# Kernel tuning notes

Hardware: AMD Instinct MI355X
Metric: run time of the kernel (lower is better)

## Reference

```python
import jax, jax.numpy as jnp
import numpy as np

B, SQ, SK, D = 8, 2048, 2048, 256

def setup_inputs() -> dict:
    key = jax.random.key(0)
    ks = jax.random.split(key, 8)
    x1 = jax.random.normal(ks[0], (B, SQ, D), dtype=jnp.float32)
    x2 = jax.random.normal(ks[1], (B, SK, D), dtype=jnp.float32)
    x3 = jax.random.normal(ks[2], (B, SK, D), dtype=jnp.float32)  # unused by the original forward (value=x3 is dead)
    mask = jax.random.bernoulli(ks[3], 0.8, (B, SK))
    scale = 0.02
    Wq = jax.random.normal(ks[4], (D, D), dtype=jnp.float32) * scale
    Wk = jax.random.normal(ks[5], (D, D), dtype=jnp.float32) * scale
    Wv = jax.random.normal(ks[6], (D, D), dtype=jnp.float32) * scale
    bq = jnp.zeros((D,), jnp.float32)
    bk = jnp.zeros((D,), jnp.float32)
    bv = jnp.zeros((D,), jnp.float32)
    return {"x1": x1, "x2": x2, "x3": x3, "Wq": Wq, "Wk": Wk, "Wv": Wv,
            "bq": bq, "bk": bk, "bv": bv, "mask": mask}

def reference(x1, x2, x3, Wq, Wk, Wv, bq, bk, bv, mask):
    d = x1.shape[-1]
    inv_sqrt_d = 1.0 / jnp.sqrt(jnp.asarray(d, x1.dtype))
    # Projections (single-head MHA with query scaling, as in torch MHA internals)
    q = (x1 @ Wq + bq) * inv_sqrt_d          # [B, SQ, D]
    k = x2 @ Wk + bk                          # [B, SK, D]
    v = x2 @ Wv + bv                          # forward_value(key): value projected from key input
    # Raw scores
    qk = jnp.einsum('bqd,bkd->bqk', q, k)     # [B, SQ, SK]
    # Mask-derived per-column rescale: qk /= (mask.size(0)/mask.sum(-2))**0.5
    m = mask.astype(qk.dtype)                 # [B, SK]
    col_count = jnp.sum(m, axis=0, keepdims=True)           # [1, SK]
    factor = jnp.sqrt(jnp.asarray(mask.shape[0], qk.dtype) / col_count)  # [1, SK]
    qk = qk / factor                          # broadcast over [B, SQ, SK]; div-by-inf -> 0 where column count is 0
    attn = jax.nn.softmax(qk, axis=-1)
    # dropout is identity in eval / p=0
    out = jnp.einsum('bqk,bkd->bqd', attn, v)  # [B, SQ, D]
    return out
```

## Files before the change

kernel.cpp:

```cpp
#include <hip/hip_runtime.h>
#include <hip/hip_bf16.h>
#include <math.h>

#define B_  8
#define SQ_ 2048
#define SK_ 2048
#define D_  256
#define NSPLIT 4
#define KEYS_PER_SPLIT (SK_ / NSPLIT)
#define NT (KEYS_PER_SPLIT / 32)

typedef __attribute__((ext_vector_type(8))) short bf16x8;
typedef __attribute__((ext_vector_type(4))) float f32x4;
typedef __attribute__((ext_vector_type(4))) unsigned short u16x4;
typedef __attribute__((ext_vector_type(8))) _Float16 f16x8;

static __device__ __forceinline__ unsigned short f2bf(float f) {
    unsigned int u = __builtin_bit_cast(unsigned int, f);
    u += 0x7FFFu + ((u >> 16) & 1u);
    return (unsigned short)(u >> 16);
}

static __device__ __forceinline__ void gld_lds16(const unsigned short* g, unsigned short* l) {
    __builtin_amdgcn_global_load_lds(
        (const __attribute__((address_space(1))) unsigned int*)g,
        (__attribute__((address_space(3))) unsigned int*)l, 16, 0, 0);
}

__global__ void prep_kernel(const float* __restrict__ Wq, const float* __restrict__ Wk,
                            const float* __restrict__ Wv, const int* __restrict__ mask,
                            unsigned short* __restrict__ wT, float* __restrict__ r) {
    int bid = blockIdx.x;
    if (bid < 768) {
        int p = bid >> 8, k = bid & 255, n = threadIdx.x;
        const float* W = (p == 0 ? Wq : (p == 1 ? Wk : Wv));
        wT[(size_t)p * D_ * D_ + (size_t)n * D_ + k] = f2bf(W[(size_t)k * D_ + n]);
    } else {
        int s = (bid - 768) * 256 + threadIdx.x;
        float c = 0.f;
#pragma unroll
        for (int b = 0; b < B_; b++) c += (mask[b * SK_ + s] != 0) ? 1.f : 0.f;
        r[s] = sqrtf(c * 0.125f);
    }
}

__global__ __launch_bounds__(256) void proj_kernel(
    const float* __restrict__ x1, const float* __restrict__ x2,
    const float* __restrict__ bq, const float* __restrict__ bk, const float* __restrict__ bv,
    const unsigned short* __restrict__ wT, const float* __restrict__ r,
    unsigned short* __restrict__ qb, unsigned short* __restrict__ kb,
    unsigned short* __restrict__ vt)
{
    __shared__ unsigned short xs[64][264];
    __shared__ unsigned short wsh[256][36];
    const int tid = threadIdx.x;
    const int mt = blockIdx.x, b = blockIdx.y, p = blockIdx.z;
    const int m0 = mt * 64;
    const float* x = (p == 0 ? x1 : x2) + (size_t)b * SQ_ * D_;

#pragma unroll
    for (int i = 0; i < 16; i++) {
        int id = tid + i * 256;
        int row = id >> 6, c4 = id & 63;
        float4 v = *(const float4*)(x + (size_t)(m0 + row) * D_ + c4 * 4);
        u16x4 u;
        u.x = f2bf(v.x); u.y = f2bf(v.y); u.z = f2bf(v.z); u.w = f2bf(v.w);
        *(u16x4*)(&xs[row][c4 * 4]) = u;
    }

    const int wv = tid >> 6, lane = tid & 63, l15 = lane & 15, quad = lane >> 4;
    const unsigned short* w = wT + (size_t)p * D_ * D_ + (size_t)tid * D_;

    f32x4 acc[4][4];
#pragma unroll
    for (int a = 0; a < 4; a++)
#pragma unroll
        for (int n = 0; n < 4; n++) acc[a][n] = (f32x4){0.f, 0.f, 0.f, 0.f};

    bf16x8 Wreg[4];
#pragma unroll
    for (int j = 0; j < 4; j++) Wreg[j] = *(const bf16x8*)(w + j * 8);

    for (int c = 0; c < 8; c++) {
        __syncthreads();
#pragma unroll
        for (int j = 0; j < 4; j++) *(bf16x8*)(&wsh[tid][j * 8]) = Wreg[j];
        if (c < 7) {
#pragma unroll
            for (int j = 0; j < 4; j++) Wreg[j] = *(const bf16x8*)(w + (c + 1) * 32 + j * 8);
        }
        __syncthreads();

        bf16x8 af[4];
#pragma unroll
        for (int a = 0; a < 4; a++)
            af[a] = *(const bf16x8*)(&xs[a * 16 + l15][c * 32 + quad * 8]);
#pragma unroll
        for (int nt = 0; nt < 4; nt++) {
            bf16x8 bfr = *(const bf16x8*)(&wsh[wv * 64 + nt * 16 + l15][quad * 8]);
#pragma unroll
            for (int a = 0; a < 4; a++)
                acc[a][nt] = __builtin_amdgcn_mfma_f32_16x16x32_bf16(af[a], bfr, acc[a][nt], 0, 0, 0);
        }
    }

    const float* bias = (p == 0 ? bq : (p == 1 ? bk : bv));
    if (p == 2) {
#pragma unroll
        for (int nt = 0; nt < 4; nt++) {
            int d = wv * 64 + nt * 16 + l15;
            float bb = bias[d];
#pragma unroll
            for (int a = 0; a < 4; a++) {
                int seqb = m0 + a * 16 + quad * 4;
                u16x4 u;
#pragma unroll
                for (int g = 0; g < 4; g++) u[g] = f2bf(acc[a][nt][g] + bb);
                *(u16x4*)(vt + ((size_t)b * D_ + d) * SK_ + seqb) = u;
            }
        }
    } else {
        unsigned short* dst = (p == 0 ? qb : kb);
#pragma unroll
        for (int a = 0; a < 4; a++) {
            int seqb = m0 + a * 16 + quad * 4;
            float rv[4];
#pragma unroll
            for (int g = 0; g < 4; g++)
                rv[g] = (p == 1) ? r[seqb + g] : 0.0625f;
#pragma unroll
            for (int nt = 0; nt < 4; nt++) {
                int col = wv * 64 + nt * 16 + l15;
                float bb = bias[col];
#pragma unroll
                for (int g = 0; g < 4; g++) {
                    float v = (acc[a][nt][g] + bb) * rv[g];
                    dst[((size_t)b * SQ_ + seqb + g) * D_ + col] = f2bf(v);
                }
            }
        }
    }
}

__global__ __launch_bounds__(256, 2) void flash_kernel(
    const unsigned short* __restrict__ qb, const unsigned short* __restrict__ kb,
    const unsigned short* __restrict__ vt, _Float16* __restrict__ Op,
    float* __restrict__ lp)
{
    __shared__ unsigned short Ks[2][32 * 256];
    __shared__ unsigned short Vs[2][256 * 32];
    __shared__ unsigned short Ps[4][32][40];
    const int tid = threadIdx.x;
    const int wv = tid >> 6, lane = tid & 63, l15 = lane & 15, quad = lane >> 4;
    const int bid = blockIdx.x;
    const int g = bid & 31, q = bid >> 5;
    const int b = g >> 2, sp = g & 3;
    const int q0 = q * 128 + wv * 32;

    const unsigned short* kbb = kb + ((size_t)b * SK_ + sp * KEYS_PER_SPLIT) * D_;
    const unsigned short* vtb = vt + (size_t)b * D_ * SK_ + sp * KEYS_PER_SPLIT;

    int krow[4], kck[4], vd[4], vch[4];
#pragma unroll
    for (int i = 0; i < 4; i++) {
        int id = i * 256 + tid;
        krow[i] = id >> 5; kck[i] = (id & 31) ^ (krow[i] & 7);
        vd[i] = id >> 2;   vch[i] = id & 3;
    }

#pragma unroll
    for (int i = 0; i < 4; i++)
        gld_lds16(kbb + (size_t)krow[i] * D_ + kck[i] * 8,
                  &Ks[0][(i * 256 + wv * 64) * 8]);
#pragma unroll
    for (int i = 0; i < 4; i++)
        gld_lds16(vtb + (size_t)vd[i] * SK_ + vch[i] * 8,
                  &Vs[0][(i * 256 + wv * 64) * 8]);

    bf16x8 qf[2][8];
#pragma unroll
    for (int mt = 0; mt < 2; mt++) {
        const unsigned short* qrow = qb + ((size_t)(b * SQ_ + q0 + mt * 16 + l15)) * D_;
#pragma unroll
        for (int c = 0; c < 8; c++)
            qf[mt][c] = *(const bf16x8*)(qrow + c * 32 + quad * 8);
    }

    f32x4 o[2][16];
#pragma unroll
    for (int mt = 0; mt < 2; mt++)
#pragma unroll
        for (int n = 0; n < 16; n++) o[mt][n] = (f32x4){0.f, 0.f, 0.f, 0.f};
    float l_[2][4] = {{0.f, 0.f, 0.f, 0.f}, {0.f, 0.f, 0.f, 0.f}};

    for (int kt = 0; kt < NT; kt++) {
        const int cur = kt & 1;
        __syncthreads();
        if (kt + 1 < NT) {
            const unsigned short* kn = kbb + (size_t)(kt + 1) * 32 * D_;
            const unsigned short* vn = vtb + (size_t)(kt + 1) * 32;
#pragma unroll
            for (int i = 0; i < 4; i++)
                gld_lds16(kn + (size_t)krow[i] * D_ + kck[i] * 8,
                          &Ks[cur ^ 1][(i * 256 + wv * 64) * 8]);
#pragma unroll
            for (int i = 0; i < 4; i++)
                gld_lds16(vn + (size_t)vd[i] * SK_ + vch[i] * 8,
                          &Vs[cur ^ 1][(i * 256 + wv * 64) * 8]);
        }

        f32x4 s[2][2];
        s[0][0] = (f32x4){0.f,0.f,0.f,0.f}; s[0][1] = (f32x4){0.f,0.f,0.f,0.f};
        s[1][0] = (f32x4){0.f,0.f,0.f,0.f}; s[1][1] = (f32x4){0.f,0.f,0.f,0.f};
#pragma unroll
        for (int h = 0; h < 2; h++)
#pragma unroll
            for (int c = 0; c < 8; c++) {
                bf16x8 kf = *(const bf16x8*)(
                    &Ks[cur][(h * 16 + l15) * 256 + (((c * 4 + quad) ^ (l15 & 7)) * 8)]);
                s[0][h] = __builtin_amdgcn_mfma_f32_16x16x32_bf16(qf[0][c], kf, s[0][h], 0, 0, 0);
                s[1][h] = __builtin_amdgcn_mfma_f32_16x16x32_bf16(qf[1][c], kf, s[1][h], 0, 0, 0);
            }

#pragma unroll
        for (int mt = 0; mt < 2; mt++)
#pragma unroll
            for (int h = 0; h < 2; h++)
#pragma unroll
                for (int g2 = 0; g2 < 4; g2++) {
                    float pv = __expf(s[mt][h][g2]);
                    l_[mt][g2] += pv;
                    Ps[wv][mt * 16 + quad * 4 + g2][h * 16 + l15] = f2bf(pv);
                }
        asm volatile("s_waitcnt lgkmcnt(0)" ::: "memory");

        bf16x8 pf0 = *(const bf16x8*)(&Ps[wv][l15][quad * 8]);
        bf16x8 pf1 = *(const bf16x8*)(&Ps[wv][16 + l15][quad * 8]);

#pragma unroll
        for (int n = 0; n < 16; n++) {
            bf16x8 vf = *(const bf16x8*)(&Vs[cur][(n * 16 + l15) * 32 + quad * 8]);
            o[0][n] = __builtin_amdgcn_mfma_f32_16x16x32_bf16(pf0, vf, o[0][n], 0, 0, 0);
            o[1][n] = __builtin_amdgcn_mfma_f32_16x16x32_bf16(pf1, vf, o[1][n], 0, 0, 0);
        }
    }

#pragma unroll
    for (int mt = 0; mt < 2; mt++)
#pragma unroll
        for (int g2 = 0; g2 < 4; g2++) {
            float t = l_[mt][g2];
            t += __shfl_xor(t, 1, 64);
            t += __shfl_xor(t, 2, 64);
            t += __shfl_xor(t, 4, 64);
            t += __shfl_xor(t, 8, 64);
            l_[mt][g2] = t;
        }

    _Float16* op = Op + ((size_t)(sp * B_ + b) * SQ_ + q0) * D_;
#pragma unroll
    for (int mt = 0; mt < 2; mt++)
#pragma unroll
        for (int g2 = 0; g2 < 4; g2++) {
            size_t ro = (size_t)(mt * 16 + quad * 4 + g2) * D_ + l15;
#pragma unroll
            for (int n = 0; n < 16; n++)
                op[ro + n * 16] = (_Float16)(o[mt][n][g2]);
        }
    if (l15 == 0) {
        float* lpp = lp + (size_t)(sp * B_ + b) * SQ_ + q0;
#pragma unroll
        for (int mt = 0; mt < 2; mt++)
#pragma unroll
            for (int g2 = 0; g2 < 4; g2++)
                lpp[mt * 16 + quad * 4 + g2] = l_[mt][g2];
    }
}

__global__ __launch_bounds__(256) void combine_kernel(
    const _Float16* __restrict__ Op, const float* __restrict__ lp,
    float* __restrict__ out)
{
    const int gid = blockIdx.x * 256 + threadIdx.x;
    const int row = gid >> 5;
    const size_t base = (size_t)gid * 8;
    float l = lp[row] + lp[B_ * SQ_ + row] + lp[2 * B_ * SQ_ + row] + lp[3 * B_ * SQ_ + row];
    float inv = 1.f / l;
    float acc[8] = {0,0,0,0,0,0,0,0};
#pragma unroll
    for (int sp = 0; sp < NSPLIT; sp++) {
        f16x8 v = *(const f16x8*)(Op + (size_t)sp * B_ * SQ_ * D_ + base);
#pragma unroll
        for (int j = 0; j < 8; j++) acc[j] += (float)v[j];
    }
    float4 r0 = {acc[0] * inv, acc[1] * inv, acc[2] * inv, acc[3] * inv};
    float4 r1 = {acc[4] * inv, acc[5] * inv, acc[6] * inv, acc[7] * inv};
    *(float4*)(out + base) = r0;
    *(float4*)(out + base + 4) = r1;
}

extern "C" void kernel_launch(void* const* d_in, const int* in_sizes, int n_in,
                              void* d_out, int out_size, void* d_ws, size_t ws_size,
                              hipStream_t stream)
{
    const float* x1 = (const float*)d_in[0];
    const float* x2 = (const float*)d_in[1];
    const float* Wq = (const float*)d_in[3];
    const float* Wk = (const float*)d_in[4];
    const float* Wv = (const float*)d_in[5];
    const float* bq = (const float*)d_in[6];
    const float* bk = (const float*)d_in[7];
    const float* bv = (const float*)d_in[8];
    const int*  mask = (const int*)d_in[9];
    float* out = (float*)d_out;

    char* ws = (char*)d_ws;
    unsigned short* qb = (unsigned short*)(ws);
    unsigned short* kb = (unsigned short*)(ws + 8388608);
    unsigned short* vt = (unsigned short*)(ws + 16777216);
    unsigned short* wT = (unsigned short*)(ws + 25165824);
    float*          r  = (float*)(ws + 25559040);
    float*          lp = (float*)(ws + 25567232);
    _Float16*       Op = (_Float16*)(ws + 25829376);

    prep_kernel<<<dim3(768 + SK_ / 256), 256, 0, stream>>>(Wq, Wk, Wv, mask, wT, r);
    proj_kernel<<<dim3(SQ_ / 64, B_, 3), 256, 0, stream>>>(x1, x2, bq, bk, bv, wT, r, qb, kb, vt);
    flash_kernel<<<dim3((SQ_ / 128) * B_ * NSPLIT), 256, 0, stream>>>(qb, kb, vt, Op, lp);
    combine_kernel<<<dim3((B_ * SQ_ * D_ / 8) / 256), 256, 0, stream>>>(Op, lp, out);
}
```

Before: 188.5 us.

## Fuse split-K combine into flash kernel, load proj weights directly, swizzle V LDS

The separate combine kernel is removed. Each flash block now increments a per-(batch, q-tile) atomic counter, and the last of the four split blocks merges the partial outputs and writes the final result, which saves one kernel launch. The projection kernel drops its shared-memory weight staging and per-chunk barriers and loads B fragments from global memory straight into registers, with a one-chunk prefetch. The V tile in LDS gets an XOR swizzle to cut bank conflicts. In exchange, the reduction is serialized in the last-arriving blocks and counter init is added to the prep kernel.

```diff
diff --git a/kernel.cpp b/kernel.cpp
--- a/kernel.cpp
+++ b/kernel.cpp
@@ -29,14 +29,16 @@
 
 __global__ void prep_kernel(const float* __restrict__ Wq, const float* __restrict__ Wk,
                             const float* __restrict__ Wv, const int* __restrict__ mask,
-                            unsigned short* __restrict__ wT, float* __restrict__ r) {
-    int bid = blockIdx.x;
+                            unsigned short* __restrict__ wT, float* __restrict__ r,
+                            int* __restrict__ cnt) {
+    int bid = blockIdx.x, tid = threadIdx.x;
     if (bid < 768) {
-        int p = bid >> 8, k = bid & 255, n = threadIdx.x;
+        int p = bid >> 8, k = bid & 255;
         const float* W = (p == 0 ? Wq : (p == 1 ? Wk : Wv));
-        wT[(size_t)p * D_ * D_ + (size_t)n * D_ + k] = f2bf(W[(size_t)k * D_ + n]);
+        wT[(size_t)p * D_ * D_ + (size_t)tid * D_ + k] = f2bf(W[(size_t)k * D_ + tid]);
     } else {
-        int s = (bid - 768) * 256 + threadIdx.x;
+        if (bid == 768 && tid < 128) cnt[tid] = 0;
+        int s = (bid - 768) * 256 + tid;
         float c = 0.f;
 #pragma unroll
         for (int b = 0; b < B_; b++) c += (mask[b * SK_ + s] != 0) ? 1.f : 0.f;
@@ -52,11 +54,12 @@
     unsigned short* __restrict__ vt)
 {
     __shared__ unsigned short xs[64][264];
-    __shared__ unsigned short wsh[256][36];
     const int tid = threadIdx.x;
+    const int wv = tid >> 6, lane = tid & 63, l15 = lane & 15, quad = lane >> 4;
     const int mt = blockIdx.x, b = blockIdx.y, p = blockIdx.z;
     const int m0 = mt * 64;
     const float* x = (p == 0 ? x1 : x2) + (size_t)b * SQ_ * D_;
+    const unsigned short* wbase = wT + (size_t)p * D_ * D_;
 
 #pragma unroll
     for (int i = 0; i < 16; i++) {
@@ -68,8 +71,10 @@
         *(u16x4*)(&xs[row][c4 * 4]) = u;
     }
 
-    const int wv = tid >> 6, lane = tid & 63, l15 = lane & 15, quad = lane >> 4;
-    const unsigned short* w = wT + (size_t)p * D_ * D_ + (size_t)tid * D_;
+    bf16x8 wcur[4];
+#pragma unroll
+    for (int nt = 0; nt < 4; nt++)
+        wcur[nt] = *(const bf16x8*)(wbase + (size_t)(wv * 64 + nt * 16 + l15) * D_ + quad * 8);
 
     f32x4 acc[4][4];
 #pragma unroll
@@ -77,30 +82,29 @@
 #pragma unroll
         for (int n = 0; n < 4; n++) acc[a][n] = (f32x4){0.f, 0.f, 0.f, 0.f};
 
-    bf16x8 Wreg[4];
-#pragma unroll
-    for (int j = 0; j < 4; j++) Wreg[j] = *(const bf16x8*)(w + j * 8);
-
+    __syncthreads();
+
+#pragma unroll
     for (int c = 0; c < 8; c++) {
-        __syncthreads();
-#pragma unroll
-        for (int j = 0; j < 4; j++) *(bf16x8*)(&wsh[tid][j * 8]) = Wreg[j];
+        bf16x8 wnxt[4];
         if (c < 7) {
 #pragma unroll
-            for (int j = 0; j < 4; j++) Wreg[j] = *(const bf16x8*)(w + (c + 1) * 32 + j * 8);
-        }
-        __syncthreads();
-
+            for (int nt = 0; nt < 4; nt++)
+                wnxt[nt] = *(const bf16x8*)(wbase + (size_t)(wv * 64 + nt * 16 + l15) * D_
+                                            + (c + 1) * 32 + quad * 8);
+        }
         bf16x8 af[4];
 #pragma unroll
         for (int a = 0; a < 4; a++)
             af[a] = *(const bf16x8*)(&xs[a * 16 + l15][c * 32 + quad * 8]);
 #pragma unroll
-        for (int nt = 0; nt < 4; nt++) {
-            bf16x8 bfr = *(const bf16x8*)(&wsh[wv * 64 + nt * 16 + l15][quad * 8]);
+        for (int nt = 0; nt < 4; nt++)
 #pragma unroll
             for (int a = 0; a < 4; a++)
-                acc[a][nt] = __builtin_amdgcn_mfma_f32_16x16x32_bf16(af[a], bfr, acc[a][nt], 0, 0, 0);
+                acc[a][nt] = __builtin_amdgcn_mfma_f32_16x16x32_bf16(af[a], wcur[nt], acc[a][nt], 0, 0, 0);
+        if (c < 7) {
+#pragma unroll
+            for (int nt = 0; nt < 4; nt++) wcur[nt] = wnxt[nt];
         }
     }
 
@@ -145,11 +149,12 @@
 __global__ __launch_bounds__(256, 2) void flash_kernel(
     const unsigned short* __restrict__ qb, const unsigned short* __restrict__ kb,
     const unsigned short* __restrict__ vt, _Float16* __restrict__ Op,
-    float* __restrict__ lp)
+    float* __restrict__ lp, int* __restrict__ cnt, float* __restrict__ out)
 {
     __shared__ unsigned short Ks[2][32 * 256];
     __shared__ unsigned short Vs[2][256 * 32];
     __shared__ unsigned short Ps[4][32][40];
+    __shared__ int winner;
     const int tid = threadIdx.x;
     const int wv = tid >> 6, lane = tid & 63, l15 = lane & 15, quad = lane >> 4;
     const int bid = blockIdx.x;
@@ -165,17 +170,15 @@
     for (int i = 0; i < 4; i++) {
         int id = i * 256 + tid;
         krow[i] = id >> 5; kck[i] = (id & 31) ^ (krow[i] & 7);
-        vd[i] = id >> 2;   vch[i] = id & 3;
+        vd[i] = id >> 2;   vch[i] = (id & 3) ^ ((vd[i] >> 1) & 3);
     }
 
 #pragma unroll
     for (int i = 0; i < 4; i++)
-        gld_lds16(kbb + (size_t)krow[i] * D_ + kck[i] * 8,
-                  &Ks[0][(i * 256 + wv * 64) * 8]);
+        gld_lds16(kbb + (size_t)krow[i] * D_ + kck[i] * 8, &Ks[0][(i * 256 + wv * 64) * 8]);
 #pragma unroll
     for (int i = 0; i < 4; i++)
-        gld_lds16(vtb + (size_t)vd[i] * SK_ + vch[i] * 8,
-                  &Vs[0][(i * 256 + wv * 64) * 8]);
+        gld_lds16(vtb + (size_t)vd[i] * SK_ + vch[i] * 8, &Vs[0][(i * 256 + wv * 64) * 8]);
 
     bf16x8 qf[2][8];
 #pragma unroll
@@ -237,9 +240,10 @@
         bf16x8 pf0 = *(const bf16x8*)(&Ps[wv][l15][quad * 8]);
         bf16x8 pf1 = *(const bf16x8*)(&Ps[wv][16 + l15][quad * 8]);
 
+        const int vsw = ((quad ^ ((l15 >> 1) & 3)) * 8);
 #pragma unroll
         for (int n = 0; n < 16; n++) {
-            bf16x8 vf = *(const bf16x8*)(&Vs[cur][(n * 16 + l15) * 32 + quad * 8]);
+            bf16x8 vf = *(const bf16x8*)(&Vs[cur][(n * 16 + l15) * 32 + vsw]);
             o[0][n] = __builtin_amdgcn_mfma_f32_16x16x32_bf16(pf0, vf, o[0][n], 0, 0, 0);
             o[1][n] = __builtin_amdgcn_mfma_f32_16x16x32_bf16(pf1, vf, o[1][n], 0, 0, 0);
         }
@@ -275,28 +279,36 @@
             for (int g2 = 0; g2 < 4; g2++)
                 lpp[mt * 16 + quad * 4 + g2] = l_[mt][g2];
     }
-}
-
-__global__ __launch_bounds__(256) void combine_kernel(
-    const _Float16* __restrict__ Op, const float* __restrict__ lp,
-    float* __restrict__ out)
-{
-    const int gid = blockIdx.x * 256 + threadIdx.x;
-    const int row = gid >> 5;
-    const size_t base = (size_t)gid * 8;
-    float l = lp[row] + lp[B_ * SQ_ + row] + lp[2 * B_ * SQ_ + row] + lp[3 * B_ * SQ_ + row];
-    float inv = 1.f / l;
-    float acc[8] = {0,0,0,0,0,0,0,0};
-#pragma unroll
-    for (int sp = 0; sp < NSPLIT; sp++) {
-        f16x8 v = *(const f16x8*)(Op + (size_t)sp * B_ * SQ_ * D_ + base);
-#pragma unroll
-        for (int j = 0; j < 8; j++) acc[j] += (float)v[j];
-    }
-    float4 r0 = {acc[0] * inv, acc[1] * inv, acc[2] * inv, acc[3] * inv};
-    float4 r1 = {acc[4] * inv, acc[5] * inv, acc[6] * inv, acc[7] * inv};
-    *(float4*)(out + base) = r0;
-    *(float4*)(out + base + 4) = r1;
+
+    __threadfence();
+    if (tid == 0) winner = (atomicAdd(cnt + (b * 16 + q), 1) == NSPLIT - 1);
+    __syncthreads();
+    if (!winner) return;
+    __threadfence();
+
+    const int rows0 = q * 128;
+    for (int it = 0; it < 16; it++) {
+        int task = it * 256 + tid;
+        int row = task >> 5, ch = task & 31;
+        size_t lrow = (size_t)b * SQ_ + rows0 + row;
+        float l = 0.f;
+#pragma unroll
+        for (int sp2 = 0; sp2 < NSPLIT; sp2++)
+            l += lp[(size_t)sp2 * B_ * SQ_ + lrow];
+        float inv = 1.f / l;
+        float acc2[8] = {0,0,0,0,0,0,0,0};
+#pragma unroll
+        for (int sp2 = 0; sp2 < NSPLIT; sp2++) {
+            f16x8 v = *(const f16x8*)(Op + ((size_t)sp2 * B_ * SQ_ + lrow) * D_ + ch * 8);
+#pragma unroll
+            for (int j = 0; j < 8; j++) acc2[j] += (float)v[j];
+        }
+        float* op2 = out + lrow * D_ + ch * 8;
+        float4 r0 = {acc2[0] * inv, acc2[1] * inv, acc2[2] * inv, acc2[3] * inv};
+        float4 r1 = {acc2[4] * inv, acc2[5] * inv, acc2[6] * inv, acc2[7] * inv};
+        *(float4*)(op2) = r0;
+        *(float4*)(op2 + 4) = r1;
+    }
 }
 
 extern "C" void kernel_launch(void* const* d_in, const int* in_sizes, int n_in,
@@ -322,9 +334,9 @@
     float*          r  = (float*)(ws + 25559040);
     float*          lp = (float*)(ws + 25567232);
     _Float16*       Op = (_Float16*)(ws + 25829376);
-
-    prep_kernel<<<dim3(768 + SK_ / 256), 256, 0, stream>>>(Wq, Wk, Wv, mask, wT, r);
+    int*            cnt = (int*)(ws + 59383808);
+
+    prep_kernel<<<dim3(768 + SK_ / 256), 256, 0, stream>>>(Wq, Wk, Wv, mask, wT, r, cnt);
     proj_kernel<<<dim3(SQ_ / 64, B_, 3), 256, 0, stream>>>(x1, x2, bq, bk, bv, wT, r, qb, kb, vt);
-    flash_kernel<<<dim3((SQ_ / 128) * B_ * NSPLIT), 256, 0, stream>>>(qb, kb, vt, Op, lp);
-    combine_kernel<<<dim3((B_ * SQ_ * D_ / 8) / 256), 256, 0, stream>>>(Op, lp, out);
-}
+    flash_kernel<<<dim3((SQ_ / 128) * B_ * NSPLIT), 256, 0, stream>>>(qb, kb, vt, Op, lp, cnt, out);
+}
```

Measured after the change: 314.8 us. +67.0%, slower.
